# Kernel tuning notes

Hardware: AMD Instinct MI355X
Metric: run time of the kernel (lower is better)

## Reference

```python
import jax, jax.numpy as jnp
import numpy as np

S, N, M = 8, 4096, 64          # snapshots, atoms, total neighbors (sum of max_num_neighs)
L = 20.0                        # periodic box length
R_CS, R_C = 2.0, 6.0            # smooth cutoff radii
DSUB = 16                       # dim_sub_net
PAD_FRAC = 0.15                 # fraction of -1 padded neighbor slots


def _mlp(x, params):
    # DenseChainNet: Linear -> relu between layers, no activation after last layer
    n = len(params)
    for i, (W, b) in enumerate(params):
        x = x @ W + b
        if i < n - 1:
            x = jax.nn.relu(x)
    return x


def _lin(k, fan_in, fan_out):
    k1, k2 = jax.random.split(k)
    s = 1.0 / np.sqrt(fan_in)
    W = jax.random.uniform(k1, (fan_in, fan_out), minval=-s, maxval=s, dtype=jnp.float32)
    b = jax.random.uniform(k2, (fan_out,), minval=-s, maxval=s, dtype=jnp.float32)
    return W, b


def setup_inputs() -> dict:
    key = jax.random.key(0)
    ks = jax.random.split(key, 12)
    inputs = jax.random.uniform(ks[0], (S, N, 3), dtype=jnp.float32) * L
    input_types = jax.random.randint(ks[1], (S, N), 0, 2)
    # neighbor indices, guaranteed != self, with -1 padding
    base = jnp.arange(N, dtype=jnp.int32)[None, :, None]
    off = jax.random.randint(ks[2], (S, N, M), 1, N)
    neigh = (base + off) % N
    pad = jax.random.uniform(ks[3], (S, N, M)) < PAD_FRAC
    neigh_list = jnp.where(pad, -1, neigh).astype(jnp.int32)
    es1_w, es1_b = _lin(ks[4], 2, 4)
    es2_w, es2_b = _lin(ks[5], 4, 4)
    fs1_w, fs1_b = _lin(ks[6], 4, 4)
    fs2_w, fs2_b = _lin(ks[7], 4, 4)
    en1_w, en1_b = _lin(ks[8], 4, 8)
    en2_w, en2_b = _lin(ks[9], 8, 16)
    en3_w, en3_b = _lin(ks[10], 16, 32)
    return dict(inputs=inputs, input_types=input_types, neigh_list=neigh_list,
                es1_w=es1_w, es1_b=es1_b, es2_w=es2_w, es2_b=es2_b,
                fs1_w=fs1_w, fs1_b=fs1_b, fs2_w=fs2_w, fs2_b=fs2_b,
                en1_w=en1_w, en1_b=en1_b, en2_w=en2_w, en2_b=en2_b,
                en3_w=en3_w, en3_b=en3_b)


def reference(inputs, input_types, neigh_list,
              es1_w, es1_b, es2_w, es2_b,
              fs1_w, fs1_b, fs2_w, fs2_b,
              en1_w, en1_b, en2_w, en2_b, en3_w, en3_b):
    mask = neigh_list == -1                               # [S,N,M]
    idx = jnp.where(mask, 0, neigh_list)
    flat = idx.reshape(S, N * M)
    # gather neighbor coordinates with periodic minimum-image convention
    pos_j = jnp.take_along_axis(inputs, flat[..., None], axis=1).reshape(S, N, M, 3)
    d = pos_j - inputs[:, :, None, :]
    d = d - L * jnp.round(d / L)
    r = jnp.sqrt(jnp.sum(d * d, axis=-1) + 1e-12)         # [S,N,M]
    # smooth cutoff: s(r) = 1/r for r<r_cs, cosine switch to 0 at r_c
    u = (r - R_CS) / (R_C - R_CS)
    sw = jnp.where(r < R_CS, 1.0,
                   jnp.where(r < R_C, 0.5 * jnp.cos(jnp.pi * u) + 0.5, 0.0))
    s_ij = jnp.where(mask, 0.0, sw / r)                   # [S,N,M]
    r_ij = d * (s_ij / r)[..., None]                      # s(r) * d / r, [S,N,M,3]
    # species pair descriptor (symmetrized over pair order)
    neigh_types = jnp.take_along_axis(input_types, flat, axis=1).reshape(S, N, M)
    self_t = jnp.broadcast_to(input_types[:, :, None], (S, N, M))
    pairs = jnp.stack([self_t, neigh_types], axis=-1).astype(jnp.float32).reshape(-1, 2)
    es = [(es1_w, es1_b), (es2_w, es2_b)]
    td = _mlp(pairs, es) + _mlp(pairs[:, ::-1], es)
    td = _mlp(td, [(fs1_w, fs1_b), (fs2_w, fs2_b)]).reshape(S, N, M, -1)  # [S,N,M,4]
    s_tilde = (td * s_ij[..., None]).reshape(S * N * M, -1)
    G = _mlp(s_tilde, [(en1_w, en1_b), (en2_w, en2_b), (en3_w, en3_b)]).reshape(S, N, M, -1)  # [S,N,M,32]
    r_tilde = jnp.concatenate([s_ij[..., None], r_ij], axis=-1)            # [S,N,M,4]
    R = jnp.einsum('snmd,snmk->sndk', r_tilde, G[..., :DSUB])              # [S,N,4,16]
    R1 = jnp.einsum('snmd,sndk->snmk', r_tilde, R)                         # [S,N,M,16]
    D = jnp.einsum('snmg,snmk->sngk', G, R1)                               # [S,N,32,16]
    return D
```

## Files before the change

kernel.cpp:

```cpp
#include <hip/hip_runtime.h>
#include <math.h>

#define SS 8
#define NN 4096
#define MM 64
#define LBOX 20.0f

typedef __attribute__((ext_vector_type(8)))  short    short8;
typedef __attribute__((ext_vector_type(2)))  float    floatx2;
typedef __attribute__((ext_vector_type(4)))  float    floatx4;
typedef __attribute__((ext_vector_type(16))) float    floatx16;
typedef __attribute__((ext_vector_type(2)))  unsigned uintx2;
typedef __attribute__((ext_vector_type(2)))  __bf16   bf16x2;

__device__ inline unsigned pkbf(float a, float b) {
    bf16x2 p; p.x = (__bf16)a; p.y = (__bf16)b;
    unsigned u; __builtin_memcpy(&u, &p, 4); return u;
}
__device__ inline unsigned short bfbits(float x) {
    __bf16 b = (__bf16)x;
    unsigned short u; __builtin_memcpy(&u, &b, 2); return u;
}

__global__ __launch_bounds__(256) void desc_kernel(
    const float* __restrict__ pos,
    const int*   __restrict__ types,
    const int*   __restrict__ neigh,
    const float* __restrict__ es1_w, const float* __restrict__ es1_b,
    const float* __restrict__ es2_w, const float* __restrict__ es2_b,
    const float* __restrict__ fs1_w, const float* __restrict__ fs1_b,
    const float* __restrict__ fs2_w, const float* __restrict__ fs2_b,
    const float* __restrict__ en1_w, const float* __restrict__ en1_b,
    const float* __restrict__ en2_w, const float* __restrict__ en2_b,
    const float* __restrict__ en3_w, const float* __restrict__ en3_b,
    float* __restrict__ out)
{
    __shared__ alignas(16) unsigned short sh_W2x[2][16][8];
    __shared__ alignas(16) unsigned short sh_h2[4][16][72];
    __shared__ alignas(16) unsigned short sh_rt[4][4][72];
    __shared__ alignas(16) float sh_PT[4][4][20];
    __shared__ alignas(16) float sh_W3p[512];
    __shared__ alignas(16) float sh_b3p[16][2];
    __shared__ alignas(16) float sh_A[4][128];
    __shared__ alignas(16) float sh_vt[4][8];

    const int tid = threadIdx.x;

    if (tid < 4) {
        const float ti = (float)(tid >> 1), tj = (float)(tid & 1);
        float e[4] = {0.f, 0.f, 0.f, 0.f};
        #pragma unroll
        for (int swp = 0; swp < 2; ++swp) {
            const float a = swp ? tj : ti, b = swp ? ti : tj;
            float h[4];
            #pragma unroll
            for (int k = 0; k < 4; ++k)
                h[k] = fmaxf(a * es1_w[k] + b * es1_w[4 + k] + es1_b[k], 0.f);
            #pragma unroll
            for (int k = 0; k < 4; ++k) {
                float acc = es2_b[k];
                #pragma unroll
                for (int j = 0; j < 4; ++j) acc += h[j] * es2_w[j * 4 + k];
                e[k] += acc;
            }
        }
        float f[4];
        #pragma unroll
        for (int k = 0; k < 4; ++k) {
            float acc = fs1_b[k];
            #pragma unroll
            for (int j = 0; j < 4; ++j) acc += e[j] * fs1_w[j * 4 + k];
            f[k] = fmaxf(acc, 0.f);
        }
        float td[4];
        #pragma unroll
        for (int k = 0; k < 4; ++k) {
            float acc = fs2_b[k];
            #pragma unroll
            for (int j = 0; j < 4; ++j) acc += f[j] * fs2_w[j * 4 + k];
            td[k] = acc;
        }
        #pragma unroll
        for (int o = 0; o < 8; ++o) {
            float acc = 0.f;
            #pragma unroll
            for (int d = 0; d < 4; ++d) acc += td[d] * en1_w[d * 8 + o];
            sh_vt[tid][o] = acc;
        }
    }
    {
        const int q = tid >> 7, col = (tid >> 3) & 15, j = tid & 7;
        const float wv = q ? (j == 0 ? en2_b[col] : 0.f) : en2_w[j * 16 + col];
        sh_W2x[q][col][j] = bfbits(wv);
    }
    #pragma unroll
    for (int rr = 0; rr < 2; ++rr) {
        const int i = tid + rr * 256;
        const int hp = i >> 6, g = (i >> 2) & 15, w = i & 3;
        sh_W3p[i] = en3_w[(2 * hp + (w >> 1)) * 32 + g + 16 * (w & 1)];
    }
    if (tid < 32) sh_b3p[tid >> 1][tid & 1] = en3_b[(tid & 1) * 16 + (tid >> 1)];
    __syncthreads();

    const int wave = __builtin_amdgcn_readfirstlane(tid >> 6);
    const int lane = tid & 63;
    const int atom = __builtin_amdgcn_readfirstlane(blockIdx.x * 4 + (tid >> 6));
    const int sbase = atom & ~(NN - 1);

    const float xi = pos[atom * 3 + 0];
    const float yi = pos[atom * 3 + 1];
    const float zi = pos[atom * 3 + 2];
    const int   ti = types[atom];

    const int nb  = neigh[atom * MM + lane];
    const int msk = nb < 0;
    const int gj  = sbase + (msk ? 0 : nb);

    const float* pj = pos + gj * 3;
    float dx = pj[0] - xi;
    float dy = pj[1] - yi;
    float dz = pj[2] - zi;
    dx -= LBOX * rintf(dx * (1.0f / LBOX));
    dy -= LBOX * rintf(dy * (1.0f / LBOX));
    dz -= LBOX * rintf(dz * (1.0f / LBOX));
    const float r2   = fmaf(dx, dx, fmaf(dy, dy, fmaf(dz, dz, 1e-12f)));
    const float rinv = rsqrtf(r2);
    const float r    = r2 * rinv;
    const float u    = fminf(fmaxf((r - 2.0f) * 0.25f, 0.0f), 1.0f);
    const float swv  = 0.5f * __cosf(3.14159265358979323846f * u) + 0.5f;
    const float sij   = msk ? 0.0f : swv * rinv;
    const float scale = sij * rinv;

    const int tj = types[gj];
    const int tt = ti * 2 + tj;

    unsigned hp[4];
    {
        const float4 va = *(const float4*)(&sh_vt[tt][0]);
        const float4 vb = *(const float4*)(&sh_vt[tt][4]);
        const float h0 = fmaxf(fmaf(sij, va.x, en1_b[0]), 0.f);
        const float h1v= fmaxf(fmaf(sij, va.y, en1_b[1]), 0.f);
        const float h2v= fmaxf(fmaf(sij, va.z, en1_b[2]), 0.f);
        const float h3 = fmaxf(fmaf(sij, va.w, en1_b[3]), 0.f);
        const float h4 = fmaxf(fmaf(sij, vb.x, en1_b[4]), 0.f);
        const float h5 = fmaxf(fmaf(sij, vb.y, en1_b[5]), 0.f);
        const float h6 = fmaxf(fmaf(sij, vb.z, en1_b[6]), 0.f);
        const float h7 = fmaxf(fmaf(sij, vb.w, en1_b[7]), 0.f);
        hp[0] = pkbf(h0, h1v); hp[1] = pkbf(h2v, h3);
        hp[2] = pkbf(h4, h5);  hp[3] = pkbf(h6, h7);
    }

    const int q2 = lane >> 5;
    union U { unsigned u[4]; short8 v; } a0, a1;
    #pragma unroll
    for (int i = 0; i < 4; ++i) {
        const unsigned other = (unsigned)__shfl_xor((int)hp[i], 32, 64);
        const unsigned bias  = (i == 0) ? 0x3F80u : 0u;
        a0.u[i] = q2 ? bias : hp[i];
        a1.u[i] = q2 ? bias : other;
    }
    const short8 bw = *(const short8*)&sh_W2x[q2][lane & 15][0];
    floatx16 c0 = {}, c1 = {};
    c0 = __builtin_amdgcn_mfma_f32_32x32x16_bf16(a0.v, bw, c0, 0, 0, 0);
    c1 = __builtin_amdgcn_mfma_f32_32x32x16_bf16(a1.v, bw, c1, 0, 0, 0);

    const int col32 = lane & 31;
    if (col32 < 16) {
        unsigned short* row = &sh_h2[wave][col32][0];
        #pragma unroll
        for (int g = 0; g < 4; ++g) {
            const int m = 8 * g + 4 * q2;
            uintx2 w0, w1;
            w0.x = pkbf(fmaxf(c0[4*g+0], 0.f), fmaxf(c0[4*g+1], 0.f));
            w0.y = pkbf(fmaxf(c0[4*g+2], 0.f), fmaxf(c0[4*g+3], 0.f));
            *(uintx2*)(row + m) = w0;
            w1.x = pkbf(fmaxf(c1[4*g+0], 0.f), fmaxf(c1[4*g+1], 0.f));
            w1.y = pkbf(fmaxf(c1[4*g+2], 0.f), fmaxf(c1[4*g+3], 0.f));
            *(uintx2*)(row + 32 + m) = w1;
        }
    }
    {
        const unsigned p0 = pkbf(sij, dx * scale), p1 = pkbf(dy * scale, dz * scale);
        sh_rt[wave][0][lane] = (unsigned short)p0;
        sh_rt[wave][1][lane] = (unsigned short)(p0 >> 16);
        sh_rt[wave][2][lane] = (unsigned short)p1;
        sh_rt[wave][3][lane] = (unsigned short)(p1 >> 16);
    }
    asm volatile("s_waitcnt lgkmcnt(0)" ::: "memory");

    const int col16 = lane & 15;
    const int q4    = lane >> 4;
    const int m0    = q4 * 8;
    floatx4 cP = {0.f, 0.f, 0.f, 0.f};
    floatx4 cQ = {0.f, 0.f, 0.f, 0.f};
    const short8 ones = (short8)(short)0x3F80;
    #pragma unroll
    for (int ck = 0; ck < 2; ++ck) {
        const short8 af = *(const short8*)&sh_h2[wave][col16][ck * 32 + m0];
        const short8 bf = *(const short8*)&sh_rt[wave][col16 & 3][ck * 32 + m0];
        cP = __builtin_amdgcn_mfma_f32_16x16x32_bf16(af, bf, cP, 0, 0, 0);
        cQ = __builtin_amdgcn_mfma_f32_16x16x32_bf16(ones, bf, cQ, 0, 0, 0);
    }
    if (col16 < 4) *(floatx4*)&sh_PT[wave][col16][q4 * 4] = cP;
    const float qd = cQ[0];
    asm volatile("s_waitcnt lgkmcnt(0)" ::: "memory");

    {
        const int g0 = lane >> 2, dd = lane & 3;
        const floatx2 b3v = *(const floatx2*)&sh_b3p[g0][0];
        floatx2 acc2 = floatx2{qd, qd} * b3v;
        #pragma unroll
        for (int h4 = 0; h4 < 4; ++h4) {
            const floatx4 pv = *(const floatx4*)&sh_PT[wave][dd][h4 * 4];
            const floatx4 wa = *(const floatx4*)&sh_W3p[(h4 * 2 + 0) * 64 + g0 * 4];
            const floatx4 wb = *(const floatx4*)&sh_W3p[(h4 * 2 + 1) * 64 + g0 * 4];
            acc2 += floatx2{pv.x, pv.x} * floatx2{wa.x, wa.y};
            acc2 += floatx2{pv.y, pv.y} * floatx2{wa.z, wa.w};
            acc2 += floatx2{pv.z, pv.z} * floatx2{wb.x, wb.y};
            acc2 += floatx2{pv.w, pv.w} * floatx2{wb.z, wb.w};
        }
        sh_A[wave][lane]      = acc2.x;
        sh_A[wave][lane + 64] = acc2.y;
    }
    asm volatile("s_waitcnt lgkmcnt(0)" ::: "memory");

    {
        const int g = lane >> 1, koff = (lane & 1) * 8;
        const floatx4 Ag = *(const floatx4*)&sh_A[wave][g * 4];
        floatx4 o0, o1;
        #pragma unroll
        for (int jj = 0; jj < 8; ++jj) {
            const floatx4 Ak = *(const floatx4*)&sh_A[wave][(koff + jj) * 4];
            const float v = fmaf(Ag.x, Ak.x, fmaf(Ag.y, Ak.y, fmaf(Ag.z, Ak.z, Ag.w * Ak.w)));
            if (jj < 4) o0[jj] = v; else o1[jj - 4] = v;
        }
        float* op = out + (size_t)atom * 512 + lane * 8;
        __builtin_nontemporal_store(o0, (floatx4*)op);
        __builtin_nontemporal_store(o1, (floatx4*)(op + 4));
    }
}

extern "C" void kernel_launch(void* const* d_in, const int* in_sizes, int n_in,
                              void* d_out, int out_size, void* d_ws, size_t ws_size,
                              hipStream_t stream) {
    const float* pos   = (const float*)d_in[0];
    const int*   typ   = (const int*)d_in[1];
    const int*   ngh   = (const int*)d_in[2];
    desc_kernel<<<dim3((SS * NN) / 4), dim3(256), 0, stream>>>(
        pos, typ, ngh,
        (const float*)d_in[3],  (const float*)d_in[4],
        (const float*)d_in[5],  (const float*)d_in[6],
        (const float*)d_in[7],  (const float*)d_in[8],
        (const float*)d_in[9],  (const float*)d_in[10],
        (const float*)d_in[11], (const float*)d_in[12],
        (const float*)d_in[13], (const float*)d_in[14],
        (const float*)d_in[15], (const float*)d_in[16],
        (float*)d_out);
}
```

Baseline: 133.0 us.

## Process four atoms per wave with prefetched neighbor gathers and scalar en2 layer

Each wave now loops over four atoms instead of one, with the grid shrunk to match, so the per-block weight staging is amortized over more work. The next atom's neighbor indices, positions and types are prefetched while the current atom is computed, to hide gather latency. The second embedding layer is replaced: instead of a bf16 MFMA with a shuffle and an extra LDS weight table, each lane runs a scalar FMA loop reading en2 weights from global memory. The trade-off is more VALU work per lane and fewer blocks in flight, which may reduce latency hiding across waves.

Result: no change. 133.6 us (+0.4%).

```diff
diff --git a/kernel.cpp b/kernel.cpp
--- a/kernel.cpp
+++ b/kernel.cpp
@@ -9,17 +9,11 @@
 typedef __attribute__((ext_vector_type(8)))  short    short8;
 typedef __attribute__((ext_vector_type(2)))  float    floatx2;
 typedef __attribute__((ext_vector_type(4)))  float    floatx4;
-typedef __attribute__((ext_vector_type(16))) float    floatx16;
-typedef __attribute__((ext_vector_type(2)))  unsigned uintx2;
 typedef __attribute__((ext_vector_type(2)))  __bf16   bf16x2;
 
 __device__ inline unsigned pkbf(float a, float b) {
     bf16x2 p; p.x = (__bf16)a; p.y = (__bf16)b;
     unsigned u; __builtin_memcpy(&u, &p, 4); return u;
-}
-__device__ inline unsigned short bfbits(float x) {
-    __bf16 b = (__bf16)x;
-    unsigned short u; __builtin_memcpy(&u, &b, 2); return u;
 }
 
 __global__ __launch_bounds__(256) void desc_kernel(
@@ -35,7 +29,6 @@
     const float* __restrict__ en3_w, const float* __restrict__ en3_b,
     float* __restrict__ out)
 {
-    __shared__ alignas(16) unsigned short sh_W2x[2][16][8];
     __shared__ alignas(16) unsigned short sh_h2[4][16][72];
     __shared__ alignas(16) unsigned short sh_rt[4][4][72];
     __shared__ alignas(16) float sh_PT[4][4][20];
@@ -87,11 +80,6 @@
             for (int d = 0; d < 4; ++d) acc += td[d] * en1_w[d * 8 + o];
             sh_vt[tid][o] = acc;
         }
-    }
-    {
-        const int q = tid >> 7, col = (tid >> 3) & 15, j = tid & 7;
-        const float wv = q ? (j == 0 ? en2_b[col] : 0.f) : en2_w[j * 16 + col];
-        sh_W2x[q][col][j] = bfbits(wv);
     }
     #pragma unroll
     for (int rr = 0; rr < 2; ++rr) {
@@ -102,141 +90,141 @@
     if (tid < 32) sh_b3p[tid >> 1][tid & 1] = en3_b[(tid & 1) * 16 + (tid >> 1)];
     __syncthreads();
 
-    const int wave = __builtin_amdgcn_readfirstlane(tid >> 6);
+    const int wave = tid >> 6;
     const int lane = tid & 63;
-    const int atom = __builtin_amdgcn_readfirstlane(blockIdx.x * 4 + (tid >> 6));
-    const int sbase = atom & ~(NN - 1);
-
-    const float xi = pos[atom * 3 + 0];
-    const float yi = pos[atom * 3 + 1];
-    const float zi = pos[atom * 3 + 2];
-    const int   ti = types[atom];
-
-    const int nb  = neigh[atom * MM + lane];
-    const int msk = nb < 0;
-    const int gj  = sbase + (msk ? 0 : nb);
-
-    const float* pj = pos + gj * 3;
-    float dx = pj[0] - xi;
-    float dy = pj[1] - yi;
-    float dz = pj[2] - zi;
-    dx -= LBOX * rintf(dx * (1.0f / LBOX));
-    dy -= LBOX * rintf(dy * (1.0f / LBOX));
-    dz -= LBOX * rintf(dz * (1.0f / LBOX));
-    const float r2   = fmaf(dx, dx, fmaf(dy, dy, fmaf(dz, dz, 1e-12f)));
-    const float rinv = rsqrtf(r2);
-    const float r    = r2 * rinv;
-    const float u    = fminf(fmaxf((r - 2.0f) * 0.25f, 0.0f), 1.0f);
-    const float swv  = 0.5f * __cosf(3.14159265358979323846f * u) + 0.5f;
-    const float sij   = msk ? 0.0f : swv * rinv;
-    const float scale = sij * rinv;
-
-    const int tj = types[gj];
-    const int tt = ti * 2 + tj;
-
-    unsigned hp[4];
-    {
-        const float4 va = *(const float4*)(&sh_vt[tt][0]);
-        const float4 vb = *(const float4*)(&sh_vt[tt][4]);
-        const float h0 = fmaxf(fmaf(sij, va.x, en1_b[0]), 0.f);
-        const float h1v= fmaxf(fmaf(sij, va.y, en1_b[1]), 0.f);
-        const float h2v= fmaxf(fmaf(sij, va.z, en1_b[2]), 0.f);
-        const float h3 = fmaxf(fmaf(sij, va.w, en1_b[3]), 0.f);
-        const float h4 = fmaxf(fmaf(sij, vb.x, en1_b[4]), 0.f);
-        const float h5 = fmaxf(fmaf(sij, vb.y, en1_b[5]), 0.f);
-        const float h6 = fmaxf(fmaf(sij, vb.z, en1_b[6]), 0.f);
-        const float h7 = fmaxf(fmaf(sij, vb.w, en1_b[7]), 0.f);
-        hp[0] = pkbf(h0, h1v); hp[1] = pkbf(h2v, h3);
-        hp[2] = pkbf(h4, h5);  hp[3] = pkbf(h6, h7);
-    }
-
-    const int q2 = lane >> 5;
-    union U { unsigned u[4]; short8 v; } a0, a1;
+    const int atomBase = blockIdx.x * 16 + wave * 4;
+    const int sbase = atomBase & ~(NN - 1);
+
+    int   nb_c = neigh[atomBase * MM + lane];
+    int   gj_c = sbase + (nb_c < 0 ? 0 : nb_c);
+    float px_c = pos[gj_c * 3 + 0];
+    float py_c = pos[gj_c * 3 + 1];
+    float pz_c = pos[gj_c * 3 + 2];
+    int   tj_c = types[gj_c];
+
     #pragma unroll
-    for (int i = 0; i < 4; ++i) {
-        const unsigned other = (unsigned)__shfl_xor((int)hp[i], 32, 64);
-        const unsigned bias  = (i == 0) ? 0x3F80u : 0u;
-        a0.u[i] = q2 ? bias : hp[i];
-        a1.u[i] = q2 ? bias : other;
-    }
-    const short8 bw = *(const short8*)&sh_W2x[q2][lane & 15][0];
-    floatx16 c0 = {}, c1 = {};
-    c0 = __builtin_amdgcn_mfma_f32_32x32x16_bf16(a0.v, bw, c0, 0, 0, 0);
-    c1 = __builtin_amdgcn_mfma_f32_32x32x16_bf16(a1.v, bw, c1, 0, 0, 0);
-
-    const int col32 = lane & 31;
-    if (col32 < 16) {
-        unsigned short* row = &sh_h2[wave][col32][0];
-        #pragma unroll
-        for (int g = 0; g < 4; ++g) {
-            const int m = 8 * g + 4 * q2;
-            uintx2 w0, w1;
-            w0.x = pkbf(fmaxf(c0[4*g+0], 0.f), fmaxf(c0[4*g+1], 0.f));
-            w0.y = pkbf(fmaxf(c0[4*g+2], 0.f), fmaxf(c0[4*g+3], 0.f));
-            *(uintx2*)(row + m) = w0;
-            w1.x = pkbf(fmaxf(c1[4*g+0], 0.f), fmaxf(c1[4*g+1], 0.f));
-            w1.y = pkbf(fmaxf(c1[4*g+2], 0.f), fmaxf(c1[4*g+3], 0.f));
-            *(uintx2*)(row + 32 + m) = w1;
-        }
-    }
-    {
-        const unsigned p0 = pkbf(sij, dx * scale), p1 = pkbf(dy * scale, dz * scale);
-        sh_rt[wave][0][lane] = (unsigned short)p0;
-        sh_rt[wave][1][lane] = (unsigned short)(p0 >> 16);
-        sh_rt[wave][2][lane] = (unsigned short)p1;
-        sh_rt[wave][3][lane] = (unsigned short)(p1 >> 16);
-    }
-    asm volatile("s_waitcnt lgkmcnt(0)" ::: "memory");
-
-    const int col16 = lane & 15;
-    const int q4    = lane >> 4;
-    const int m0    = q4 * 8;
-    floatx4 cP = {0.f, 0.f, 0.f, 0.f};
-    floatx4 cQ = {0.f, 0.f, 0.f, 0.f};
-    const short8 ones = (short8)(short)0x3F80;
-    #pragma unroll
-    for (int ck = 0; ck < 2; ++ck) {
-        const short8 af = *(const short8*)&sh_h2[wave][col16][ck * 32 + m0];
-        const short8 bf = *(const short8*)&sh_rt[wave][col16 & 3][ck * 32 + m0];
-        cP = __builtin_amdgcn_mfma_f32_16x16x32_bf16(af, bf, cP, 0, 0, 0);
-        cQ = __builtin_amdgcn_mfma_f32_16x16x32_bf16(ones, bf, cQ, 0, 0, 0);
-    }
-    if (col16 < 4) *(floatx4*)&sh_PT[wave][col16][q4 * 4] = cP;
-    const float qd = cQ[0];
-    asm volatile("s_waitcnt lgkmcnt(0)" ::: "memory");
-
-    {
-        const int g0 = lane >> 2, dd = lane & 3;
-        const floatx2 b3v = *(const floatx2*)&sh_b3p[g0][0];
-        floatx2 acc2 = floatx2{qd, qd} * b3v;
-        #pragma unroll
-        for (int h4 = 0; h4 < 4; ++h4) {
-            const floatx4 pv = *(const floatx4*)&sh_PT[wave][dd][h4 * 4];
-            const floatx4 wa = *(const floatx4*)&sh_W3p[(h4 * 2 + 0) * 64 + g0 * 4];
-            const floatx4 wb = *(const floatx4*)&sh_W3p[(h4 * 2 + 1) * 64 + g0 * 4];
-            acc2 += floatx2{pv.x, pv.x} * floatx2{wa.x, wa.y};
-            acc2 += floatx2{pv.y, pv.y} * floatx2{wa.z, wa.w};
-            acc2 += floatx2{pv.z, pv.z} * floatx2{wb.x, wb.y};
-            acc2 += floatx2{pv.w, pv.w} * floatx2{wb.z, wb.w};
-        }
-        sh_A[wave][lane]      = acc2.x;
-        sh_A[wave][lane + 64] = acc2.y;
-    }
-    asm volatile("s_waitcnt lgkmcnt(0)" ::: "memory");
-
-    {
-        const int g = lane >> 1, koff = (lane & 1) * 8;
-        const floatx4 Ag = *(const floatx4*)&sh_A[wave][g * 4];
-        floatx4 o0, o1;
-        #pragma unroll
-        for (int jj = 0; jj < 8; ++jj) {
-            const floatx4 Ak = *(const floatx4*)&sh_A[wave][(koff + jj) * 4];
-            const float v = fmaf(Ag.x, Ak.x, fmaf(Ag.y, Ak.y, fmaf(Ag.z, Ak.z, Ag.w * Ak.w)));
-            if (jj < 4) o0[jj] = v; else o1[jj - 4] = v;
-        }
-        float* op = out + (size_t)atom * 512 + lane * 8;
-        __builtin_nontemporal_store(o0, (floatx4*)op);
-        __builtin_nontemporal_store(o1, (floatx4*)(op + 4));
+    for (int a = 0; a < 4; ++a) {
+        const int atom = atomBase + a;
+        const int   nb  = nb_c;
+        const float pxx = px_c, pyy = py_c, pzz = pz_c;
+        const int   tjv = tj_c;
+
+        int nb_n = 0;
+        if (a < 3) nb_n = neigh[(atom + 1) * MM + lane];
+
+        const float xi = pos[atom * 3 + 0];
+        const float yi = pos[atom * 3 + 1];
+        const float zi = pos[atom * 3 + 2];
+        const int   ti = types[atom];
+
+        const int msk = nb < 0;
+        float dx = pxx - xi;
+        float dy = pyy - yi;
+        float dz = pzz - zi;
+        dx -= LBOX * rintf(dx * (1.0f / LBOX));
+        dy -= LBOX * rintf(dy * (1.0f / LBOX));
+        dz -= LBOX * rintf(dz * (1.0f / LBOX));
+        const float r2   = fmaf(dx, dx, fmaf(dy, dy, fmaf(dz, dz, 1e-12f)));
+        const float rinv = rsqrtf(r2);
+        const float r    = r2 * rinv;
+        const float u    = fminf(fmaxf((r - 2.0f) * 0.25f, 0.0f), 1.0f);
+        const float swv  = 0.5f * __cosf(3.14159265358979323846f * u) + 0.5f;
+        const float sij   = msk ? 0.0f : swv * rinv;
+        const float scale = sij * rinv;
+        const int   tt    = ti * 2 + tjv;
+
+        float h1[8];
+        {
+            const float4 va = *(const float4*)(&sh_vt[tt][0]);
+            const float4 vb = *(const float4*)(&sh_vt[tt][4]);
+            h1[0] = fmaxf(fmaf(sij, va.x, en1_b[0]), 0.f);
+            h1[1] = fmaxf(fmaf(sij, va.y, en1_b[1]), 0.f);
+            h1[2] = fmaxf(fmaf(sij, va.z, en1_b[2]), 0.f);
+            h1[3] = fmaxf(fmaf(sij, va.w, en1_b[3]), 0.f);
+            h1[4] = fmaxf(fmaf(sij, vb.x, en1_b[4]), 0.f);
+            h1[5] = fmaxf(fmaf(sij, vb.y, en1_b[5]), 0.f);
+            h1[6] = fmaxf(fmaf(sij, vb.z, en1_b[6]), 0.f);
+            h1[7] = fmaxf(fmaf(sij, vb.w, en1_b[7]), 0.f);
+        }
+
+        #pragma unroll
+        for (int k = 0; k < 16; ++k) {
+            float acc = en2_b[k];
+            #pragma unroll
+            for (int i = 0; i < 8; ++i) acc = fmaf(h1[i], en2_w[i * 16 + k], acc);
+            const unsigned pk = pkbf(fmaxf(acc, 0.f), 0.f);
+            sh_h2[wave][k][lane] = (unsigned short)pk;
+        }
+        {
+            const unsigned p0 = pkbf(sij, dx * scale), p1 = pkbf(dy * scale, dz * scale);
+            sh_rt[wave][0][lane] = (unsigned short)p0;
+            sh_rt[wave][1][lane] = (unsigned short)(p0 >> 16);
+            sh_rt[wave][2][lane] = (unsigned short)p1;
+            sh_rt[wave][3][lane] = (unsigned short)(p1 >> 16);
+        }
+
+        if (a < 3) {
+            gj_c = sbase + (nb_n < 0 ? 0 : nb_n);
+            px_c = pos[gj_c * 3 + 0];
+            py_c = pos[gj_c * 3 + 1];
+            pz_c = pos[gj_c * 3 + 2];
+            tj_c = types[gj_c];
+            nb_c = nb_n;
+        }
+
+        asm volatile("s_waitcnt lgkmcnt(0)" ::: "memory");
+
+        const int col16 = lane & 15;
+        const int q4    = lane >> 4;
+        const int m0    = q4 * 8;
+        floatx4 cP = {0.f, 0.f, 0.f, 0.f};
+        floatx4 cQ = {0.f, 0.f, 0.f, 0.f};
+        const short8 ones = (short8)(short)0x3F80;
+        #pragma unroll
+        for (int ck = 0; ck < 2; ++ck) {
+            const short8 af = *(const short8*)&sh_h2[wave][col16][ck * 32 + m0];
+            const short8 bf = *(const short8*)&sh_rt[wave][col16 & 3][ck * 32 + m0];
+            cP = __builtin_amdgcn_mfma_f32_16x16x32_bf16(af, bf, cP, 0, 0, 0);
+            cQ = __builtin_amdgcn_mfma_f32_16x16x32_bf16(ones, bf, cQ, 0, 0, 0);
+        }
+        if (col16 < 4) *(floatx4*)&sh_PT[wave][col16][q4 * 4] = cP;
+        const float qd = cQ[0];
+        asm volatile("s_waitcnt lgkmcnt(0)" ::: "memory");
+
+        {
+            const int g0 = lane >> 2, dd = lane & 3;
+            const floatx2 b3v = *(const floatx2*)&sh_b3p[g0][0];
+            floatx2 acc2 = floatx2{qd, qd} * b3v;
+            #pragma unroll
+            for (int h4 = 0; h4 < 4; ++h4) {
+                const floatx4 pv = *(const floatx4*)&sh_PT[wave][dd][h4 * 4];
+                const floatx4 wa = *(const floatx4*)&sh_W3p[(h4 * 2 + 0) * 64 + g0 * 4];
+                const floatx4 wb = *(const floatx4*)&sh_W3p[(h4 * 2 + 1) * 64 + g0 * 4];
+                acc2 += floatx2{pv.x, pv.x} * floatx2{wa.x, wa.y};
+                acc2 += floatx2{pv.y, pv.y} * floatx2{wa.z, wa.w};
+                acc2 += floatx2{pv.z, pv.z} * floatx2{wb.x, wb.y};
+                acc2 += floatx2{pv.w, pv.w} * floatx2{wb.z, wb.w};
+            }
+            sh_A[wave][lane]      = acc2.x;
+            sh_A[wave][lane + 64] = acc2.y;
+        }
+        asm volatile("s_waitcnt lgkmcnt(0)" ::: "memory");
+
+        {
+            const int g = lane >> 1, koff = (lane & 1) * 8;
+            const floatx4 Ag = *(const floatx4*)&sh_A[wave][g * 4];
+            floatx4 o0, o1;
+            #pragma unroll
+            for (int jj = 0; jj < 8; ++jj) {
+                const floatx4 Ak = *(const floatx4*)&sh_A[wave][(koff + jj) * 4];
+                const float v = fmaf(Ag.x, Ak.x, fmaf(Ag.y, Ak.y, fmaf(Ag.z, Ak.z, Ag.w * Ak.w)));
+                if (jj < 4) o0[jj] = v; else o1[jj - 4] = v;
+            }
+            float* op = out + (size_t)atom * 512 + lane * 8;
+            __builtin_nontemporal_store(o0, (floatx4*)op);
+            __builtin_nontemporal_store(o1, (floatx4*)(op + 4));
+        }
+        asm volatile("s_waitcnt lgkmcnt(0)" ::: "memory");
     }
 }
 
@@ -246,7 +234,7 @@
     const float* pos   = (const float*)d_in[0];
     const int*   typ   = (const int*)d_in[1];
     const int*   ngh   = (const int*)d_in[2];
-    desc_kernel<<<dim3((SS * NN) / 4), dim3(256), 0, stream>>>(
+    desc_kernel<<<dim3((SS * NN) / 16), dim3(256), 0, stream>>>(
         pos, typ, ngh,
         (const float*)d_in[3],  (const float*)d_in[4],
         (const float*)d_in[5],  (const float*)d_in[6],
```
